# Kernel optimization log

Hardware: AMD Instinct MI355X
Metric: run time of the kernel (lower is better)

Reference implementation:

```python
import jax, jax.numpy as jnp
import numpy as np

B, L, D, H = 4, 2048, 1024, 16
HD = D // H
NEG = -1e9  # stands in for -inf in masks; identical softmax result, grad-safe
EPS = 1e-5


def _layer_norm(x, g, b):
    mu = jnp.mean(x, axis=-1, keepdims=True)
    var = jnp.mean((x - mu) ** 2, axis=-1, keepdims=True)
    return (x - mu) * jax.lax.rsqrt(var + EPS) * g + b


def setup_inputs() -> dict:
    key = jax.random.key(0)
    ks = jax.random.split(key, 8)
    x = jax.random.normal(ks[0], (B, L, D), dtype=jnp.float32)
    # length-based padding: valid lengths in [L//2, L]; True = padded position
    lengths = jax.random.randint(ks[1], (B,), L // 2, L + 1)
    padding_mask = jnp.arange(L)[None, :] >= lengths[:, None]  # (B, L) bool
    # additive causal mask: 0 on/below diagonal, NEG above
    causal_mask = jnp.where(jnp.tril(jnp.ones((L, L), dtype=bool)), 0.0, NEG).astype(jnp.float32)

    def linear_params(k, fan_in, fan_out):
        bound = float(np.sqrt(6.0 / (fan_in + fan_out)))  # xavier_uniform
        W = jax.random.uniform(k, (fan_out, fan_in), jnp.float32, -bound, bound)
        b = jnp.zeros((fan_out,), jnp.float32)
        return W, b

    Wq, bq = linear_params(ks[2], D, D)
    Wk, bk = linear_params(ks[3], D, D)
    Wv, bv = linear_params(ks[4], D, D)
    Wo, bo = linear_params(ks[5], D, D)
    g_pre = jnp.ones((D,), jnp.float32); b_pre = jnp.zeros((D,), jnp.float32)
    g_ln = jnp.ones((D,), jnp.float32); b_ln = jnp.zeros((D,), jnp.float32)
    return {
        "x": x, "padding_mask": padding_mask, "causal_mask": causal_mask,
        "Wq": Wq, "bq": bq, "Wk": Wk, "bk": bk, "Wv": Wv, "bv": bv,
        "Wo": Wo, "bo": bo, "g_pre": g_pre, "b_pre": b_pre,
        "g_ln": g_ln, "b_ln": b_ln,
    }


def reference(x, padding_mask, causal_mask, Wq, bq, Wk, bk, Wv, bv, Wo, bo,
              g_pre, b_pre, g_ln, b_ln):
    # pre-LayerNorm (residual uses the normed x, matching the torch code)
    h = _layer_norm(x, g_pre, b_pre)  # (B, L, D)

    def heads(W, b):
        y = jnp.einsum('bld,ed->ble', h, W) + b           # torch Linear: x @ W.T + b
        return y.reshape(B, L, H, HD).transpose(0, 2, 1, 3)  # (B, H, L, HD)

    q, k, v = heads(Wq, bq), heads(Wk, bk), heads(Wv, bv)

    scores = jnp.einsum('bhld,bhmd->bhlm', q, k) / jnp.sqrt(jnp.float32(HD))
    scores = scores + causal_mask  # additive causal mask broadcast over (B, H)
    # padding mask: True = masked key position
    scores = jnp.where(padding_mask[:, None, None, :], NEG, scores)
    attn = jax.nn.softmax(scores, axis=-1)  # dropout p=0.0 (eval / disabled)

    out = jnp.einsum('bhlm,bhmd->bhld', attn, v)          # (B, H, L, HD)
    out = out.transpose(0, 2, 1, 3).reshape(B, L, D)
    out = jnp.einsum('bld,ed->ble', out, Wo) + bo
    return _layer_norm(out + h, g_ln, b_ln)
```

## Files before the change

kernel.cpp:

```cpp
#include <hip/hip_runtime.h>


#define Bq 4
#define Lq 2048
#define Dq 1024
#define Hq 16
#define HDq 64
#define Mq (Bq * Lq)

typedef __attribute__((ext_vector_type(8))) short short8;
typedef __attribute__((ext_vector_type(4))) float f32x4;
typedef __attribute__((address_space(3))) unsigned char lds_byte;
typedef __attribute__((address_space(1))) unsigned char gbl_byte;

__device__ __forceinline__ unsigned short f2b(float f) {
    unsigned int u = __float_as_uint(f);
    unsigned int r = (u + 0x7fffu + ((u >> 16) & 1u)) >> 16;
    return (unsigned short)r;
}
__device__ __forceinline__ float b2f(unsigned short u) {
    return __uint_as_float(((unsigned int)u) << 16);
}
__device__ __forceinline__ unsigned int packbf(float lo, float hi) {
    return (unsigned int)f2b(lo) | ((unsigned int)f2b(hi) << 16);
}

#define GLL16(gsrc, ldst)                                              \
    __builtin_amdgcn_global_load_lds((const gbl_byte*)(gsrc),          \
                                     (lds_byte*)(ldst), 16, 0, 0)

#define MFMA_BF16(A, B, C) \
    __builtin_amdgcn_mfma_f32_16x16x32_bf16((A), (B), (C), 0, 0, 0)

__global__ void setup_kernel(const unsigned char* __restrict__ m8,
                             int* __restrict__ lengths) {
    __shared__ int bad;
    __shared__ int fo[4];
    const int tid = threadIdx.x;
    if (tid == 0) bad = 0;
    if (tid < 4) fo[tid] = Lq;
    __syncthreads();
    for (int i = tid; i < Bq * Lq; i += 256) {
        unsigned char v = m8[i];
        if (v) {
            int r = i >> 11, c = i & (Lq - 1);
            atomicMin(&fo[r], c);
            if (c < Lq / 2) atomicOr(&bad, 1);
            else if (c < Lq - 1 && m8[i + 1] == 0) atomicOr(&bad, 1);
        }
    }
    __syncthreads();
    int anyone = (fo[0] < Lq) | (fo[1] < Lq) | (fo[2] < Lq) | (fo[3] < Lq);
    bool use8 = (bad == 0) && anyone;
    if (!use8) {
        __syncthreads();
        if (tid < 4) fo[tid] = Lq;
        __syncthreads();
        const int* m32 = (const int*)m8;
        for (int i = tid; i < Bq * Lq; i += 256) {
            if (m32[i] != 0) atomicMin(&fo[i >> 11], i & (Lq - 1));
        }
        __syncthreads();
    }
    if (tid < 4) lengths[tid] = fo[tid];
}

__global__ __launch_bounds__(256) void cvt4_kernel(
    const float* __restrict__ s0, const float* __restrict__ s1,
    const float* __restrict__ s2, const float* __restrict__ s3,
    unsigned short* __restrict__ dst) {
    const int region = blockIdx.x >> 10;
    const int i = (blockIdx.x & 1023) * 256 + threadIdx.x;
    const float* src = (region == 0) ? s0 : (region == 1) ? s1
                       : (region == 2) ? s2 : s3;
    float4 v = ((const float4*)src)[i];
    ushort4 o;
    o.x = f2b(v.x); o.y = f2b(v.y); o.z = f2b(v.z); o.w = f2b(v.w);
    ((ushort4*)dst)[(size_t)region * (Dq * Dq / 4) + i] = o;
}

__global__ __launch_bounds__(256) void ln_pre_kernel(
    const float* __restrict__ x, const float* __restrict__ g,
    const float* __restrict__ bb, unsigned short* __restrict__ out) {
    const int row = blockIdx.x, tid = threadIdx.x;
    float4 u = ((const float4*)x)[(size_t)row * 256 + tid];
    float s = u.x + u.y + u.z + u.w;
    float ss = u.x * u.x + u.y * u.y + u.z * u.z + u.w * u.w;
#pragma unroll
    for (int off = 32; off > 0; off >>= 1) {
        s += __shfl_xor(s, off);
        ss += __shfl_xor(ss, off);
    }
    __shared__ float sred[4], ssred[4];
    const int w = tid >> 6, lane = tid & 63;
    if (lane == 0) { sred[w] = s; ssred[w] = ss; }
    __syncthreads();
    s = sred[0] + sred[1] + sred[2] + sred[3];
    ss = ssred[0] + ssred[1] + ssred[2] + ssred[3];
    const float mean = s * (1.f / Dq);
    const float rstd = rsqrtf(ss * (1.f / Dq) - mean * mean + 1e-5f);
    float4 gv = ((const float4*)g)[tid];
    float4 bv = ((const float4*)bb)[tid];
    ushort4 o;
    o.x = f2b((u.x - mean) * rstd * gv.x + bv.x);
    o.y = f2b((u.y - mean) * rstd * gv.y + bv.y);
    o.z = f2b((u.z - mean) * rstd * gv.z + bv.z);
    o.w = f2b((u.w - mean) * rstd * gv.w + bv.w);
    ((ushort4*)out)[(size_t)row * 256 + tid] = o;
}

__global__ __launch_bounds__(256) void qkv_gemm_kernel(
    const unsigned short* __restrict__ A, const unsigned short* __restrict__ W3,
    const float* __restrict__ bq, const float* __restrict__ bk,
    const float* __restrict__ bv, unsigned short* __restrict__ Qo,
    unsigned short* __restrict__ Ko, unsigned short* __restrict__ Vto) {
    __shared__ unsigned short As[128][32];
    __shared__ unsigned short Bs[128][32];
    const int tid = threadIdx.x;
    const int w = tid >> 6, lane = tid & 63;
    const int lm = lane & 15, lq = lane >> 4;
    const int m0 = blockIdx.y << 7, n0 = blockIdx.x << 7;
    const int wm = (w >> 1) << 6, wn = (w & 1) << 6;
    f32x4 acc[4][4];
#pragma unroll
    for (int i = 0; i < 4; ++i)
#pragma unroll
        for (int j = 0; j < 4; ++j) acc[i][j] = (f32x4){0.f, 0.f, 0.f, 0.f};
    for (int k0 = 0; k0 < Dq; k0 += 32) {
        __syncthreads();
#pragma unroll
        for (int j = 0; j < 2; ++j) {
            const int base = j * 256 + w * 64;
            const int slot = base + lane;
            const int row = slot >> 2, c = slot & 3;
            GLL16(A + (size_t)(m0 + row) * Dq + k0 + c * 8,
                  (unsigned short*)As + base * 8);
            GLL16(W3 + (size_t)(n0 + row) * Dq + k0 + c * 8,
                  (unsigned short*)Bs + base * 8);
        }
        __syncthreads();
        short8 af[4], bf[4];
#pragma unroll
        for (int t = 0; t < 4; ++t)
            af[t] = *(const short8*)&As[wm + t * 16 + lm][lq * 8];
#pragma unroll
        for (int t = 0; t < 4; ++t)
            bf[t] = *(const short8*)&Bs[wn + t * 16 + lm][lq * 8];
#pragma unroll
        for (int mt = 0; mt < 4; ++mt)
#pragma unroll
            for (int nt = 0; nt < 4; ++nt)
                acc[mt][nt] = __builtin_amdgcn_mfma_f32_16x16x32_bf16(
                    af[mt], bf[nt], acc[mt][nt], 0, 0, 0);
    }
    const int region = n0 >> 10;
    const float* bias = (region == 0) ? bq : (region == 1) ? bk : bv;
    const float scale = (region == 0) ? 0.125f : 1.0f;
    const int nb = n0 & 1023;
#pragma unroll
    for (int nt = 0; nt < 4; ++nt) {
        const int colb = nb + wn + nt * 16 + lm;
        const float bval = bias[colb];
#pragma unroll
        for (int mt = 0; mt < 4; ++mt) {
            const int row0 = m0 + wm + mt * 16 + lq * 4;
            const int bidx = row0 >> 11, l0r = row0 & (Lq - 1);
            if (region < 2) {
                unsigned short* dst = (region == 0) ? Qo : Ko;
#pragma unroll
                for (int r = 0; r < 4; ++r)
                    dst[((size_t)(bidx * Hq + (colb >> 6)) * Lq + l0r + r) *
                            HDq + (colb & 63)] =
                        f2b((acc[mt][nt][r] + bval) * scale);
            } else {
                ushort4 o;
                o.x = f2b(acc[mt][nt][0] + bval);
                o.y = f2b(acc[mt][nt][1] + bval);
                o.z = f2b(acc[mt][nt][2] + bval);
                o.w = f2b(acc[mt][nt][3] + bval);
                *(ushort4*)&Vto[((size_t)(bidx * Hq + (colb >> 6)) * HDq +
                                 (colb & 63)) * Lq + l0r] = o;
            }
        }
    }
}

__global__ __launch_bounds__(256) void proj_gemm_kernel(
    const unsigned short* __restrict__ A, const unsigned short* __restrict__ Bw,
    const float* __restrict__ bias, float* __restrict__ Cout) {
    __shared__ unsigned short As[128][32];
    __shared__ unsigned short Bs[128][32];
    const int tid = threadIdx.x;
    const int w = tid >> 6, lane = tid & 63;
    const int lm = lane & 15, lq = lane >> 4;
    const int m0 = blockIdx.y << 7, n0 = blockIdx.x << 7;
    const int wm = (w >> 1) << 6, wn = (w & 1) << 6;
    f32x4 acc[4][4];
#pragma unroll
    for (int i = 0; i < 4; ++i)
#pragma unroll
        for (int j = 0; j < 4; ++j) acc[i][j] = (f32x4){0.f, 0.f, 0.f, 0.f};
    for (int k0 = 0; k0 < Dq; k0 += 32) {
        __syncthreads();
#pragma unroll
        for (int j = 0; j < 2; ++j) {
            const int base = j * 256 + w * 64;
            const int slot = base + lane;
            const int row = slot >> 2, c = slot & 3;
            const int rr = m0 + row, kk = k0 + c * 8;
            GLL16(A + ((size_t)((rr >> 11) * Hq + (kk >> 6)) * Lq +
                       (rr & (Lq - 1))) * HDq + (kk & 63),
                  (unsigned short*)As + base * 8);
            GLL16(Bw + (size_t)(n0 + row) * Dq + k0 + c * 8,
                  (unsigned short*)Bs + base * 8);
        }
        __syncthreads();
        short8 af[4], bf[4];
#pragma unroll
        for (int t = 0; t < 4; ++t)
            af[t] = *(const short8*)&As[wm + t * 16 + lm][lq * 8];
#pragma unroll
        for (int t = 0; t < 4; ++t)
            bf[t] = *(const short8*)&Bs[wn + t * 16 + lm][lq * 8];
#pragma unroll
        for (int mt = 0; mt < 4; ++mt)
#pragma unroll
            for (int nt = 0; nt < 4; ++nt)
                acc[mt][nt] = __builtin_amdgcn_mfma_f32_16x16x32_bf16(
                    af[mt], bf[nt], acc[mt][nt], 0, 0, 0);
    }
#pragma unroll
    for (int nt = 0; nt < 4; ++nt) {
        const float bval = bias[n0 + wn + nt * 16 + lm];
#pragma unroll
        for (int mt = 0; mt < 4; ++mt)
#pragma unroll
            for (int r = 0; r < 4; ++r)
                Cout[(size_t)(m0 + wm + mt * 16 + lq * 4 + r) * Dq + n0 + wn +
                     nt * 16 + lm] = acc[mt][nt][r] + bval;
    }
}


#define ATTN_KT_BODY(KT, KF, KFN)                                           \
    {                                                                       \
        const int kb = (KT) << 6;                                           \
        short8 vf[4][2];                                                    \
        _Pragma("unroll")                                                   \
        for (int t = 0; t < 4; ++t) {                                       \
            _Pragma("unroll")                                               \
            for (int kh = 0; kh < 2; ++kh)                                  \
                vf[t][kh] = *(const short8*)(Vb +                           \
                    (size_t)(t * 16 + lm) * Lq + kb + kh * 32 + lq * 8);    \
        }                                                                   \
        if ((KT) + 1 < nkt) {                                               \
            const int kb2 = kb + 64;                                        \
            _Pragma("unroll")                                               \
            for (int t = 0; t < 4; ++t) {                                   \
                _Pragma("unroll")                                           \
                for (int h = 0; h < 2; ++h)                                 \
                    KFN[t][h] = *(const short8*)(Kg + hb +                  \
                        (size_t)(kb2 + t * 16 + lm) * HDq + h * 32 +        \
                        lq * 8);                                            \
            }                                                               \
        }                                                                   \
        _Pragma("unroll")                                                   \
        for (int s = 0; s < 2; ++s) {                                       \
            f32x4 sc[4];                                                    \
            __builtin_amdgcn_s_setprio(1);                                  \
            _Pragma("unroll")                                               \
            for (int t = 0; t < 4; ++t) {                                   \
                f32x4 z = (f32x4){0.f, 0.f, 0.f, 0.f};                      \
                z = MFMA_BF16(KF[t][0], qf[s][0], z);                       \
                z = MFMA_BF16(KF[t][1], qf[s][1], z);                       \
                sc[t] = z;                                                  \
            }                                                               \
            __builtin_amdgcn_s_setprio(0);                                  \
            const int qmin = l0 + w * 32 + s * 16;                          \
            float pvv[16];                                                  \
            float mx = -1e30f;                                              \
            if ((kb + 63 <= qmin) && (kb + 63 < len)) {                     \
                _Pragma("unroll")                                           \
                for (int i = 0; i < 16; ++i) {                              \
                    const float v = sc[i >> 2][i & 3];                      \
                    pvv[i] = v;                                             \
                    mx = fmaxf(mx, v);                                      \
                }                                                           \
            } else {                                                        \
                const int qq = qmin + lm;                                   \
                _Pragma("unroll")                                           \
                for (int t = 0; t < 4; ++t) {                               \
                    _Pragma("unroll")                                       \
                    for (int r = 0; r < 4; ++r) {                           \
                        const int key = kb + t * 16 + lq * 4 + r;           \
                        float v = sc[t][r];                                 \
                        if (key > qq || key >= len) v = -1e30f;             \
                        pvv[t * 4 + r] = v;                                 \
                        mx = fmaxf(mx, v);                                  \
                    }                                                       \
                }                                                           \
            }                                                               \
            mx = fmaxf(mx, __shfl_xor(mx, 16));                            \
            mx = fmaxf(mx, __shfl_xor(mx, 32));                            \
            const float mnew = fmaxf(m_i[s], mx);                          \
            float psum = 0.f;                                               \
            _Pragma("unroll")                                               \
            for (int i = 0; i < 16; ++i) {                                  \
                const float p = __expf(pvv[i] - mnew);                      \
                pvv[i] = p;                                                 \
                psum += p;                                                  \
            }                                                               \
            _Pragma("unroll")                                               \
            for (int t = 0; t < 4; ++t) {                                   \
                uint2 uu;                                                   \
                uu.x = packbf(pvv[t * 4 + 0], pvv[t * 4 + 1]);              \
                uu.y = packbf(pvv[t * 4 + 2], pvv[t * 4 + 3]);              \
                *(uint2*)&Ps[w][lm][t * 16 + lq * 4] = uu;                  \
            }                                                               \
            psum += __shfl_xor(psum, 16);                                   \
            psum += __shfl_xor(psum, 32);                                   \
            const float alpha = __expf(m_i[s] - mnew);                      \
            m_i[s] = mnew;                                                  \
            l_i[s] = l_i[s] * alpha + psum;                                 \
            _Pragma("unroll")                                               \
            for (int t = 0; t < 4; ++t) {                                   \
                oacc[s][t][0] *= alpha;                                     \
                oacc[s][t][1] *= alpha;                                     \
                oacc[s][t][2] *= alpha;                                     \
                oacc[s][t][3] *= alpha;                                     \
            }                                                               \
            asm volatile("s_waitcnt lgkmcnt(0)" ::: "memory");              \
            short8 pf0 = *(const short8*)&Ps[w][lm][lq * 8];                \
            short8 pf1 = *(const short8*)&Ps[w][lm][32 + lq * 8];           \
            __builtin_amdgcn_s_setprio(1);                                  \
            _Pragma("unroll")                                               \
            for (int t = 0; t < 4; ++t) {                                   \
                oacc[s][t] = MFMA_BF16(vf[t][0], pf0, oacc[s][t]);          \
                oacc[s][t] = MFMA_BF16(vf[t][1], pf1, oacc[s][t]);          \
            }                                                               \
            __builtin_amdgcn_s_setprio(0);                                  \
        }                                                                   \
    }

__global__ __launch_bounds__(256, 2) void attn_kernel(
    const unsigned short* __restrict__ Qg, const unsigned short* __restrict__ Kg,
    const unsigned short* __restrict__ Vtg, const int* __restrict__ lengths,
    unsigned short* __restrict__ Og) {
    __shared__ unsigned short Ps[4][16][72];
    const int bx = blockIdx.x;
    const int hh = blockIdx.y, b = blockIdx.z;
    const int tid = threadIdx.x, w = tid >> 6, lane = tid & 63;
    const int lm = lane & 15, lq = lane >> 4;
    const int len = lengths[b];
    const int mxk = (len + 63) >> 6;
    const size_t hb = (size_t)(b * Hq + hh) * Lq * HDq;
    const unsigned short* Vb = Vtg + hb;

#pragma unroll
    for (int pass = 0; pass < 2; ++pass) {
        const int qt = pass ? bx : (15 - bx);
        const int l0 = qt << 7;
        short8 qf[2][2];
#pragma unroll
        for (int s = 0; s < 2; ++s)
#pragma unroll
            for (int h = 0; h < 2; ++h)
                qf[s][h] = *(const short8*)(Qg + hb +
                    (size_t)(l0 + w * 32 + s * 16 + lm) * HDq + h * 32 + lq * 8);
        f32x4 oacc[2][4];
        float m_i[2], l_i[2];
#pragma unroll
        for (int s = 0; s < 2; ++s) {
            m_i[s] = -1e30f; l_i[s] = 0.f;
#pragma unroll
            for (int t = 0; t < 4; ++t)
                oacc[s][t] = (f32x4){0.f, 0.f, 0.f, 0.f};
        }
        int nkt = 2 * qt + 2;
        if (nkt > mxk) nkt = mxk;
        short8 kfa[4][2], kfb[4][2];
#pragma unroll
        for (int t = 0; t < 4; ++t)
#pragma unroll
            for (int h = 0; h < 2; ++h)
                kfa[t][h] = *(const short8*)(Kg + hb +
                    (size_t)(t * 16 + lm) * HDq + h * 32 + lq * 8);
        int kt = 0;
        for (;;) {
            ATTN_KT_BODY(kt, kfa, kfb);
            ++kt;
            if (kt >= nkt) break;
            ATTN_KT_BODY(kt, kfb, kfa);
            ++kt;
            if (kt >= nkt) break;
        }
#pragma unroll
        for (int s = 0; s < 2; ++s) {
            const float inv = 1.f / l_i[s];
            unsigned short* Ot =
                Og + hb + (size_t)(l0 + w * 32 + s * 16 + lm) * HDq;
#pragma unroll
            for (int t = 0; t < 4; ++t) {
                ushort4 o;
                o.x = f2b(oacc[s][t][0] * inv);
                o.y = f2b(oacc[s][t][1] * inv);
                o.z = f2b(oacc[s][t][2] * inv);
                o.w = f2b(oacc[s][t][3] * inv);
                *(ushort4*)(Ot + t * 16 + lq * 4) = o;
            }
        }
    }
}

__global__ __launch_bounds__(256) void ln_final_kernel(
    const float* __restrict__ pj, const unsigned short* __restrict__ h,
    const float* __restrict__ g, const float* __restrict__ bb,
    float* __restrict__ out) {
    const int row = blockIdx.x, tid = threadIdx.x;
    float4 a = ((const float4*)pj)[(size_t)row * 256 + tid];
    ushort4 hv = ((const ushort4*)h)[(size_t)row * 256 + tid];
    float f0 = a.x + b2f(hv.x), f1 = a.y + b2f(hv.y);
    float f2 = a.z + b2f(hv.z), f3 = a.w + b2f(hv.w);
    float s = f0 + f1 + f2 + f3;
    float ss = f0 * f0 + f1 * f1 + f2 * f2 + f3 * f3;
#pragma unroll
    for (int off = 32; off > 0; off >>= 1) {
        s += __shfl_xor(s, off);
        ss += __shfl_xor(ss, off);
    }
    __shared__ float sred[4], ssred[4];
    const int w = tid >> 6, lane = tid & 63;
    if (lane == 0) { sred[w] = s; ssred[w] = ss; }
    __syncthreads();
    s = sred[0] + sred[1] + sred[2] + sred[3];
    ss = ssred[0] + ssred[1] + ssred[2] + ssred[3];
    const float mean = s * (1.f / Dq);
    const float rstd = rsqrtf(ss * (1.f / Dq) - mean * mean + 1e-5f);
    float4 gv = ((const float4*)g)[tid];
    float4 bv = ((const float4*)bb)[tid];
    float4 o;
    o.x = (f0 - mean) * rstd * gv.x + bv.x;
    o.y = (f1 - mean) * rstd * gv.y + bv.y;
    o.z = (f2 - mean) * rstd * gv.z + bv.z;
    o.w = (f3 - mean) * rstd * gv.w + bv.w;
    ((float4*)out)[(size_t)row * 256 + tid] = o;
}

extern "C" void kernel_launch(void* const* d_in, const int* in_sizes, int n_in,
                              void* d_out, int out_size, void* d_ws,
                              size_t ws_size, hipStream_t stream) {
    const float* x = (const float*)d_in[0];
    const unsigned char* mask = (const unsigned char*)d_in[1];
    const float* Wq = (const float*)d_in[3];
    const float* bq = (const float*)d_in[4];
    const float* Wk = (const float*)d_in[5];
    const float* bk = (const float*)d_in[6];
    const float* Wv = (const float*)d_in[7];
    const float* bvv = (const float*)d_in[8];
    const float* Wo = (const float*)d_in[9];
    const float* bo = (const float*)d_in[10];
    const float* g_pre = (const float*)d_in[11];
    const float* b_pre = (const float*)d_in[12];
    const float* g_ln = (const float*)d_in[13];
    const float* b_ln = (const float*)d_in[14];

    const size_t SZ = (size_t)Mq * Dq;
    const size_t WSZ = (size_t)Dq * Dq;
    unsigned short* h = (unsigned short*)d_ws;
    unsigned short* q = h + SZ;
    unsigned short* k = q + SZ;
    unsigned short* vT = k + SZ;
    unsigned short* at = vT + SZ;
    unsigned short* W3 = at + SZ;
    unsigned short* wob = W3 + 3 * WSZ;
    float* proj = (float*)(wob + WSZ);
    int* lengths = (int*)(proj + SZ);

    setup_kernel<<<1, 256, 0, stream>>>(mask, lengths);
    cvt4_kernel<<<4096, 256, 0, stream>>>(Wq, Wk, Wv, Wo, W3);
    ln_pre_kernel<<<Mq, 256, 0, stream>>>(x, g_pre, b_pre, h);

    qkv_gemm_kernel<<<dim3(3 * Dq / 128, Mq / 128), 256, 0, stream>>>(
        h, W3, bq, bk, bvv, q, k, vT);
    attn_kernel<<<dim3(Lq / 256, Hq, Bq), 256, 0, stream>>>(q, k, vT, lengths,
                                                            at);
    proj_gemm_kernel<<<dim3(Dq / 128, Mq / 128), 256, 0, stream>>>(at, wob, bo,
                                                                   proj);
    ln_final_kernel<<<Mq, 256, 0, stream>>>(proj, h, g_ln, b_ln,
                                            (float*)d_out);
}
```

Before: 405.7 us.

## Swizzle GEMM block order and batch attention QK/softmax/PV phases per wave

The QKV and output-projection GEMMs remap the linear block index so that consecutive blocks are spread across M tiles, which changes L2 locality and the order in which blocks are dispatched. In the attention inner loop, both 16-row sub-tiles' QK MFMAs are now issued back to back, then both softmaxes run, then both PV MFMA groups run, with a single LDS wait. The P staging buffer is doubled to hold both sub-tiles. This is meant to lengthen MFMA bursts and hide the softmax and LDS latency, at the cost of more registers (sc[2][4]) and more LDS, which may reduce occupancy.

```diff
diff --git a/kernel.cpp b/kernel.cpp
--- a/kernel.cpp
+++ b/kernel.cpp
@@ -119,7 +119,9 @@
     const int tid = threadIdx.x;
     const int w = tid >> 6, lane = tid & 63;
     const int lm = lane & 15, lq = lane >> 4;
-    const int m0 = blockIdx.y << 7, n0 = blockIdx.x << 7;
+    const int lin = blockIdx.y * 24 + blockIdx.x;
+    const int swz = (lin & 7) * (1536 / 8) + (lin >> 3);
+    const int m0 = (swz / 24) << 7, n0 = (swz % 24) << 7;
     const int wm = (w >> 1) << 6, wn = (w & 1) << 6;
     f32x4 acc[4][4];
 #pragma unroll
@@ -193,7 +195,9 @@
     const int tid = threadIdx.x;
     const int w = tid >> 6, lane = tid & 63;
     const int lm = lane & 15, lq = lane >> 4;
-    const int m0 = blockIdx.y << 7, n0 = blockIdx.x << 7;
+    const int lin = blockIdx.y * 8 + blockIdx.x;
+    const int swz = (lin & 7) * (512 / 8) + (lin >> 3);
+    const int m0 = (swz >> 3) << 7, n0 = (swz & 7) << 7;
     const int wm = (w >> 1) << 6, wn = (w & 1) << 6;
     f32x4 acc[4][4];
 #pragma unroll
@@ -264,25 +268,28 @@
                         lq * 8);                                            \
             }                                                               \
         }                                                                   \
+        f32x4 sc[2][4];                                                     \
+        __builtin_amdgcn_s_setprio(1);                                      \
         _Pragma("unroll")                                                   \
         for (int s = 0; s < 2; ++s) {                                       \
-            f32x4 sc[4];                                                    \
-            __builtin_amdgcn_s_setprio(1);                                  \
             _Pragma("unroll")                                               \
             for (int t = 0; t < 4; ++t) {                                   \
                 f32x4 z = (f32x4){0.f, 0.f, 0.f, 0.f};                      \
                 z = MFMA_BF16(KF[t][0], qf[s][0], z);                       \
                 z = MFMA_BF16(KF[t][1], qf[s][1], z);                       \
-                sc[t] = z;                                                  \
-            }                                                               \
-            __builtin_amdgcn_s_setprio(0);                                  \
+                sc[s][t] = z;                                               \
+            }                                                               \
+        }                                                                   \
+        __builtin_amdgcn_s_setprio(0);                                      \
+        _Pragma("unroll")                                                   \
+        for (int s = 0; s < 2; ++s) {                                       \
             const int qmin = l0 + w * 32 + s * 16;                          \
             float pvv[16];                                                  \
             float mx = -1e30f;                                              \
             if ((kb + 63 <= qmin) && (kb + 63 < len)) {                     \
                 _Pragma("unroll")                                           \
                 for (int i = 0; i < 16; ++i) {                              \
-                    const float v = sc[i >> 2][i & 3];                      \
+                    const float v = sc[s][i >> 2][i & 3];                   \
                     pvv[i] = v;                                             \
                     mx = fmaxf(mx, v);                                      \
                 }                                                           \
@@ -293,7 +300,7 @@
                     _Pragma("unroll")                                       \
                     for (int r = 0; r < 4; ++r) {                           \
                         const int key = kb + t * 16 + lq * 4 + r;           \
-                        float v = sc[t][r];                                 \
+                        float v = sc[s][t][r];                              \
                         if (key > qq || key >= len) v = -1e30f;             \
                         pvv[t * 4 + r] = v;                                 \
                         mx = fmaxf(mx, v);                                  \
@@ -315,7 +322,7 @@
                 uint2 uu;                                                   \
                 uu.x = packbf(pvv[t * 4 + 0], pvv[t * 4 + 1]);              \
                 uu.y = packbf(pvv[t * 4 + 2], pvv[t * 4 + 3]);              \
-                *(uint2*)&Ps[w][lm][t * 16 + lq * 4] = uu;                  \
+                *(uint2*)&Ps[w][s][lm][t * 16 + lq * 4] = uu;               \
             }                                                               \
             psum += __shfl_xor(psum, 16);                                   \
             psum += __shfl_xor(psum, 32);                                   \
@@ -329,24 +336,27 @@
                 oacc[s][t][2] *= alpha;                                     \
                 oacc[s][t][3] *= alpha;                                     \
             }                                                               \
-            asm volatile("s_waitcnt lgkmcnt(0)" ::: "memory");              \
-            short8 pf0 = *(const short8*)&Ps[w][lm][lq * 8];                \
-            short8 pf1 = *(const short8*)&Ps[w][lm][32 + lq * 8];           \
-            __builtin_amdgcn_s_setprio(1);                                  \
+        }                                                                   \
+        asm volatile("s_waitcnt lgkmcnt(0)" ::: "memory");                  \
+        __builtin_amdgcn_s_setprio(1);                                      \
+        _Pragma("unroll")                                                   \
+        for (int s = 0; s < 2; ++s) {                                       \
+            short8 pf0 = *(const short8*)&Ps[w][s][lm][lq * 8];             \
+            short8 pf1 = *(const short8*)&Ps[w][s][lm][32 + lq * 8];        \
             _Pragma("unroll")                                               \
             for (int t = 0; t < 4; ++t) {                                   \
                 oacc[s][t] = MFMA_BF16(vf[t][0], pf0, oacc[s][t]);          \
                 oacc[s][t] = MFMA_BF16(vf[t][1], pf1, oacc[s][t]);          \
             }                                                               \
-            __builtin_amdgcn_s_setprio(0);                                  \
         }                                                                   \
+        __builtin_amdgcn_s_setprio(0);                                      \
     }
 
 __global__ __launch_bounds__(256, 2) void attn_kernel(
     const unsigned short* __restrict__ Qg, const unsigned short* __restrict__ Kg,
     const unsigned short* __restrict__ Vtg, const int* __restrict__ lengths,
     unsigned short* __restrict__ Og) {
-    __shared__ unsigned short Ps[4][16][72];
+    __shared__ unsigned short Ps[4][2][16][72];
     const int bx = blockIdx.x;
     const int hh = blockIdx.y, b = blockIdx.z;
     const int tid = threadIdx.x, w = tid >> 6, lane = tid & 63;
```

Measured after the change: 400.7 us. Within noise of the previous version (-1.2%).
